# Performance work log

Hardware: AMD Instinct MI355X
Metric: run time of the kernel (lower is better)

The kernel has to match this reference:

```python
import jax, jax.numpy as jnp
import numpy as np

GAMMA = 0.99      # discount_factor
LAM = 0.95        # gae_decay
CLIP = 0.2        # clipping_param
LOG_2PI = float(np.log(2.0 * np.pi))

B, T, A = 512, 2048, 16


def setup_inputs() -> dict:
    key = jax.random.key(0)
    ks = jax.random.split(key, 8)
    rewards = jax.random.normal(ks[0], (B, T), dtype=jnp.float32)
    critic_out = jax.random.normal(ks[1], (B, T + 1), dtype=jnp.float32)
    mu = jax.random.normal(ks[2], (B, T, A), dtype=jnp.float32)
    sigma = jax.random.uniform(ks[3], (B, T, A), dtype=jnp.float32) * 0.5 + 0.5
    old_mu = jax.random.normal(ks[4], (B, T, A), dtype=jnp.float32)
    old_sigma = jax.random.uniform(ks[5], (B, T, A), dtype=jnp.float32) * 0.5 + 0.5
    actions = jax.random.normal(ks[6], (B, T, A), dtype=jnp.float32)
    dones = jax.random.randint(ks[7], (B, T), 0, 2, dtype=jnp.int32)
    return {"rewards": rewards, "critic_out": critic_out, "mu": mu, "sigma": sigma,
            "old_mu": old_mu, "old_sigma": old_sigma, "actions": actions, "dones": dones}


def _normal_log_prob(x, mu, sigma):
    return -jnp.log(sigma) - 0.5 * LOG_2PI - 0.5 * jnp.square((x - mu) / sigma)


def _gae(rewards, dones_f, critic_out):
    # td_residuals: rewards + gamma * V[1:] - V[:-1]   -> [B, T]
    td = rewards + GAMMA * critic_out[:, 1:] - critic_out[:, :-1]
    b, t = rewards.shape
    # Reversed recurrence: adv[t] = td[t] + gamma*lam*(1 - done[t+1]) * adv[t+1],
    # for t = T-2 .. 0; adv[T-1] stays 0 (matches original loop bounds).
    xs = (jnp.flip(td[:, : t - 1], axis=1).T,        # [T-1, B]
          jnp.flip(dones_f[:, 1:], axis=1).T)        # [T-1, B]

    def step(carry, x):
        td_t, d_t = x
        adv = td_t + GAMMA * LAM * (1.0 - d_t) * carry
        return adv, adv

    _, advs = jax.lax.scan(step, jnp.zeros((b,), rewards.dtype), xs)
    advs = jnp.flip(advs, axis=0).T                  # [B, T-1]
    return jnp.concatenate([advs, jnp.zeros((b, 1), rewards.dtype)], axis=1)


def reference(rewards, critic_out, mu, sigma, old_mu, old_sigma, actions, dones):
    dones_f = dones.astype(rewards.dtype)
    advantages = _gae(rewards, dones_f, critic_out)          # [B, T]
    lp = _normal_log_prob(actions, mu, sigma)                # [B, T, A]
    old_lp = _normal_log_prob(actions, old_mu, old_sigma)    # [B, T, A]
    ratio = jnp.exp(lp - old_lp)
    clipped = jnp.minimum(jnp.maximum(ratio, 1.0 + CLIP), 1.0 - CLIP)
    adv = advantages[..., None]                              # broadcast over action dim
    obj = jnp.minimum(adv * ratio, adv * clipped)
    entropy = jnp.log(sigma) + 0.5 + 0.5 * LOG_2PI           # Normal entropy, [B, T, A]
    return jnp.mean(obj) + entropy
```

## Files before the change

kernel.cpp:

```cpp
#include <hip/hip_runtime.h>
#include <math.h>

#define BB 512
#define TT 2048
#define AA 16
#define NTOT (512LL * 2048LL * 16LL)
#define GAMMA 0.99f
#define GLAM  0.9405f
#define ENTC  1.4189385332046727f

#define NB2 2048

__global__ __launch_bounds__(256) void gae_kernel(
    const float* __restrict__ rewards, const float* __restrict__ vout,
    const int* __restrict__ dones, float* __restrict__ adv)
{
    const int b   = blockIdx.x;
    const int tid = threadIdx.x;
    const float* rw = rewards + (size_t)b * TT;
    const float* V  = vout    + (size_t)b * (TT + 1);
    const int*   dn = dones   + (size_t)b * TT;
    float*       av = adv     + (size_t)b * TT;

    float ak[8], bk[8];
    float SA = 1.f, SB = 0.f;
    #pragma unroll
    for (int k = 0; k < 8; ++k) {
        int u = tid * 8 + k;
        float au, bu;
        if (u == 0) { au = 0.f; bu = 0.f; }
        else {
            int t = TT - 1 - u;
            bu = rw[t] + GAMMA * V[t + 1] - V[t];
            au = GLAM * (1.f - (float)dn[t + 1]);
        }
        ak[k] = au; bk[k] = bu;
        SB = au * SB + bu;
        SA = au * SA;
    }

    const int lane = tid & 63;
    const int wave = tid >> 6;

    #pragma unroll
    for (int off = 1; off < 64; off <<= 1) {
        float pA = __shfl_up(SA, off, 64);
        float pB = __shfl_up(SB, off, 64);
        if (lane >= off) { SB = SA * pB + SB; SA = SA * pA; }
    }

    __shared__ float wA[4], wB[4];
    if (lane == 63) { wA[wave] = SA; wB[wave] = SB; }
    __syncthreads();

    float PA = 1.f, PB = 0.f;
    for (int w = 0; w < wave; ++w) {
        float aw = wA[w], bw = wB[w];
        PB = aw * PB + bw;
        PA = aw * PA;
    }

    float EA = __shfl_up(SA, 1, 64);
    float EB = __shfl_up(SB, 1, 64);
    if (lane == 0) { EA = 1.f; EB = 0.f; }

    float x = EA * PB + EB;
    #pragma unroll
    for (int k = 0; k < 8; ++k) {
        x = ak[k] * x + bk[k];
        int u = tid * 8 + k;
        av[TT - 1 - u] = x;
    }
}

__device__ __forceinline__ float obj1(float x, float m, float s,
                                      float om, float os, float ad)
{
    float rs  = __builtin_amdgcn_rcpf(s);
    float ros = __builtin_amdgcn_rcpf(os);
    float z   = (x - m) * rs;
    float zo  = (x - om) * ros;
    float d   = 0.5f * (zo * zo - z * z);
    float ratio = os * rs * __expf(d);
    return fminf(ad * ratio, ad * 0.8f);
}

__global__ __launch_bounds__(256) void obj_kernel(
    const float* __restrict__ mu, const float* __restrict__ sigma,
    const float* __restrict__ old_mu, const float* __restrict__ old_sigma,
    const float* __restrict__ actions, const float* __restrict__ adv,
    double* __restrict__ partials)
{
    const int tid = threadIdx.x;
    const size_t gthread = (size_t)blockIdx.x * 256 + tid;
    const size_t stride  = (size_t)NB2 * 256;

    const float4* m4  = (const float4*)mu;
    const float4* s4  = (const float4*)sigma;
    const float4* om4 = (const float4*)old_mu;
    const float4* os4 = (const float4*)old_sigma;
    const float4* x4  = (const float4*)actions;

    double lsum = 0.0;
    #pragma unroll 2
    for (int it = 0; it < 8; ++it) {
        size_t v = gthread + (size_t)it * stride;
        float4 m  = m4[v];
        float4 s  = s4[v];
        float4 om = om4[v];
        float4 os = os4[v];
        float4 x  = x4[v];
        float ad  = adv[v >> 2];

        float o0 = obj1(x.x, m.x, s.x, om.x, os.x, ad);
        float o1 = obj1(x.y, m.y, s.y, om.y, os.y, ad);
        float o2 = obj1(x.z, m.z, s.z, om.z, os.z, ad);
        float o3 = obj1(x.w, m.w, s.w, om.w, os.w, ad);
        lsum += (double)o0 + (double)o1 + (double)o2 + (double)o3;
    }

    #pragma unroll
    for (int off = 32; off > 0; off >>= 1)
        lsum += __shfl_down(lsum, off, 64);

    __shared__ double wsum[4];
    const int lane = tid & 63, wave = tid >> 6;
    if (lane == 0) wsum[wave] = lsum;
    __syncthreads();
    if (tid == 0)
        partials[blockIdx.x] = wsum[0] + wsum[1] + wsum[2] + wsum[3];
}

__global__ __launch_bounds__(256) void reduce_kernel(
    const double* __restrict__ partials, float* __restrict__ meanOut)
{
    const int tid = threadIdx.x;
    double s = 0.0;
    for (int i = tid; i < NB2; i += 256) s += partials[i];
    #pragma unroll
    for (int off = 32; off > 0; off >>= 1)
        s += __shfl_down(s, off, 64);
    __shared__ double wsum[4];
    const int lane = tid & 63, wave = tid >> 6;
    if (lane == 0) wsum[wave] = s;
    __syncthreads();
    if (tid == 0) {
        double total = wsum[0] + wsum[1] + wsum[2] + wsum[3];
        meanOut[0] = (float)(total / (double)NTOT);
    }
}

__global__ __launch_bounds__(256) void out_kernel(
    const float* __restrict__ sigma, const float* __restrict__ meanPtr,
    float* __restrict__ out)
{
    const size_t v = (size_t)blockIdx.x * 256 + threadIdx.x;
    const float mean = *meanPtr;
    float4 s = ((const float4*)sigma)[v];
    float4 o;
    o.x = mean + __logf(s.x) + ENTC;
    o.y = mean + __logf(s.y) + ENTC;
    o.z = mean + __logf(s.z) + ENTC;
    o.w = mean + __logf(s.w) + ENTC;
    ((float4*)out)[v] = o;
}

extern "C" void kernel_launch(void* const* d_in, const int* in_sizes, int n_in,
                              void* d_out, int out_size, void* d_ws, size_t ws_size,
                              hipStream_t stream) {
    const float* rewards   = (const float*)d_in[0];
    const float* critic    = (const float*)d_in[1];
    const float* mu        = (const float*)d_in[2];
    const float* sigma     = (const float*)d_in[3];
    const float* old_mu    = (const float*)d_in[4];
    const float* old_sigma = (const float*)d_in[5];
    const float* actions   = (const float*)d_in[6];
    const int*   dones     = (const int*)d_in[7];
    float* out = (float*)d_out;

    char* ws = (char*)d_ws;
    float*  meanPtr  = (float*)ws;
    double* partials = (double*)(ws + 256);
    float*  adv      = (float*)(ws + 32768);

    gae_kernel<<<BB, 256, 0, stream>>>(rewards, critic, dones, adv);
    obj_kernel<<<NB2, 256, 0, stream>>>(mu, sigma, old_mu, old_sigma,
                                        actions, adv, partials);
    reduce_kernel<<<1, 256, 0, stream>>>(partials, meanPtr);
    out_kernel<<<(int)(NTOT / 4 / 256), 256, 0, stream>>>(sigma, meanPtr, out);
}
```

Measured before the change: 344.5 us.

## Vectorize GAE loads/stores, batch obj loads upfront, float accumulation, multi-item out kernel

The GAE kernel now reads rewards, critic values and dones as float4/int4 chunks and writes advantages as two float4 stores, replacing scalar strided accesses. The objective kernel doubles the grid to 4096 blocks with four items per thread. It issues all loads before any compute to raise memory-level parallelism, and it accumulates in four float registers instead of per-item double adds. The output kernel processes four float4 per thread over the same grid. Risks: the critic rows have a stride of 2049 floats, so the float4 loads from V are misaligned, and float accumulation loses some precision before the double reduction.

```diff
diff --git a/kernel.cpp b/kernel.cpp
--- a/kernel.cpp
+++ b/kernel.cpp
@@ -5,11 +5,14 @@
 #define TT 2048
 #define AA 16
 #define NTOT (512LL * 2048LL * 16LL)
+#define NV4  (NTOT / 4)
 #define GAMMA 0.99f
 #define GLAM  0.9405f
 #define ENTC  1.4189385332046727f
 
-#define NB2 2048
+#define NB2   4096
+#define ITER2 4
+#define S2    (NB2 * 256)
 
 __global__ __launch_bounds__(256) void gae_kernel(
     const float* __restrict__ rewards, const float* __restrict__ vout,
@@ -22,17 +25,31 @@
     const int*   dn = dones   + (size_t)b * TT;
     float*       av = adv     + (size_t)b * TT;
 
+    const int tb = (TT - 8) - 8 * tid;
+
+    const float4 r0 = ((const float4*)(rw + tb))[0];
+    const float4 r1 = ((const float4*)(rw + tb))[1];
+    const float4 v0 = ((const float4*)(V  + tb))[0];
+    const float4 v1 = ((const float4*)(V  + tb))[1];
+    const float  v8 = V[tb + 8];
+    const int4   d0 = ((const int4*)(dn + tb))[0];
+    const int4   d1 = ((const int4*)(dn + tb))[1];
+    const int    d8 = (tid > 0) ? dn[tb + 8] : 0;
+
+    float r_[8] = {r0.x, r0.y, r0.z, r0.w, r1.x, r1.y, r1.z, r1.w};
+    float v_[9] = {v0.x, v0.y, v0.z, v0.w, v1.x, v1.y, v1.z, v1.w, v8};
+    int   d_[9] = {d0.x, d0.y, d0.z, d0.w, d1.x, d1.y, d1.z, d1.w, d8};
+
     float ak[8], bk[8];
     float SA = 1.f, SB = 0.f;
     #pragma unroll
     for (int k = 0; k < 8; ++k) {
-        int u = tid * 8 + k;
+        const int j = 7 - k;
         float au, bu;
-        if (u == 0) { au = 0.f; bu = 0.f; }
+        if (tid == 0 && k == 0) { au = 0.f; bu = 0.f; }
         else {
-            int t = TT - 1 - u;
-            bu = rw[t] + GAMMA * V[t + 1] - V[t];
-            au = GLAM * (1.f - (float)dn[t + 1]);
+            bu = r_[j] + GAMMA * v_[j + 1] - v_[j];
+            au = GLAM * (1.f - (float)d_[j + 1]);
         }
         ak[k] = au; bk[k] = bu;
         SB = au * SB + bu;
@@ -65,12 +82,16 @@
     if (lane == 0) { EA = 1.f; EB = 0.f; }
 
     float x = EA * PB + EB;
+    float xv[8];
     #pragma unroll
     for (int k = 0; k < 8; ++k) {
         x = ak[k] * x + bk[k];
-        int u = tid * 8 + k;
-        av[TT - 1 - u] = x;
-    }
+        xv[k] = x;
+    }
+    float4 o0 = {xv[7], xv[6], xv[5], xv[4]};
+    float4 o1 = {xv[3], xv[2], xv[1], xv[0]};
+    ((float4*)(av + tb))[0] = o0;
+    ((float4*)(av + tb))[1] = o1;
 }
 
 __device__ __forceinline__ float obj1(float x, float m, float s,
@@ -92,8 +113,7 @@
     double* __restrict__ partials)
 {
     const int tid = threadIdx.x;
-    const size_t gthread = (size_t)blockIdx.x * 256 + tid;
-    const size_t stride  = (size_t)NB2 * 256;
+    const size_t g = (size_t)blockIdx.x * 256 + tid;
 
     const float4* m4  = (const float4*)mu;
     const float4* s4  = (const float4*)sigma;
@@ -101,23 +121,28 @@
     const float4* os4 = (const float4*)old_sigma;
     const float4* x4  = (const float4*)actions;
 
-    double lsum = 0.0;
-    #pragma unroll 2
-    for (int it = 0; it < 8; ++it) {
-        size_t v = gthread + (size_t)it * stride;
-        float4 m  = m4[v];
-        float4 s  = s4[v];
-        float4 om = om4[v];
-        float4 os = os4[v];
-        float4 x  = x4[v];
-        float ad  = adv[v >> 2];
-
-        float o0 = obj1(x.x, m.x, s.x, om.x, os.x, ad);
-        float o1 = obj1(x.y, m.y, s.y, om.y, os.y, ad);
-        float o2 = obj1(x.z, m.z, s.z, om.z, os.z, ad);
-        float o3 = obj1(x.w, m.w, s.w, om.w, os.w, ad);
-        lsum += (double)o0 + (double)o1 + (double)o2 + (double)o3;
-    }
+    float4 m[ITER2], s[ITER2], om[ITER2], os[ITER2], x[ITER2];
+    float ad[ITER2];
+    #pragma unroll
+    for (int k = 0; k < ITER2; ++k) {
+        size_t v = g + (size_t)k * S2;
+        m[k]  = m4[v];
+        s[k]  = s4[v];
+        om[k] = om4[v];
+        os[k] = os4[v];
+        x[k]  = x4[v];
+        ad[k] = adv[v >> 2];
+    }
+
+    float a0 = 0.f, a1 = 0.f, a2 = 0.f, a3 = 0.f;
+    #pragma unroll
+    for (int k = 0; k < ITER2; ++k) {
+        a0 += obj1(x[k].x, m[k].x, s[k].x, om[k].x, os[k].x, ad[k]);
+        a1 += obj1(x[k].y, m[k].y, s[k].y, om[k].y, os[k].y, ad[k]);
+        a2 += obj1(x[k].z, m[k].z, s[k].z, om[k].z, os[k].z, ad[k]);
+        a3 += obj1(x[k].w, m[k].w, s[k].w, om[k].w, os[k].w, ad[k]);
+    }
+    double lsum = ((double)a0 + (double)a1) + ((double)a2 + (double)a3);
 
     #pragma unroll
     for (int off = 32; off > 0; off >>= 1)
@@ -154,15 +179,21 @@
     const float* __restrict__ sigma, const float* __restrict__ meanPtr,
     float* __restrict__ out)
 {
-    const size_t v = (size_t)blockIdx.x * 256 + threadIdx.x;
-    const float mean = *meanPtr;
-    float4 s = ((const float4*)sigma)[v];
-    float4 o;
-    o.x = mean + __logf(s.x) + ENTC;
-    o.y = mean + __logf(s.y) + ENTC;
-    o.z = mean + __logf(s.z) + ENTC;
-    o.w = mean + __logf(s.w) + ENTC;
-    ((float4*)out)[v] = o;
+    const size_t g = (size_t)blockIdx.x * 256 + threadIdx.x;
+    const float mean = meanPtr[0];
+    const float4* s4 = (const float4*)sigma;
+    float4* o4 = (float4*)out;
+    #pragma unroll
+    for (int k = 0; k < ITER2; ++k) {
+        size_t v = g + (size_t)k * S2;
+        float4 s = s4[v];
+        float4 o;
+        o.x = mean + __logf(s.x) + ENTC;
+        o.y = mean + __logf(s.y) + ENTC;
+        o.z = mean + __logf(s.z) + ENTC;
+        o.w = mean + __logf(s.w) + ENTC;
+        o4[v] = o;
+    }
 }
 
 extern "C" void kernel_launch(void* const* d_in, const int* in_sizes, int n_in,
@@ -181,11 +212,11 @@
     char* ws = (char*)d_ws;
     float*  meanPtr  = (float*)ws;
     double* partials = (double*)(ws + 256);
-    float*  adv      = (float*)(ws + 32768);
+    float*  adv      = (float*)(ws + 65536);
 
     gae_kernel<<<BB, 256, 0, stream>>>(rewards, critic, dones, adv);
     obj_kernel<<<NB2, 256, 0, stream>>>(mu, sigma, old_mu, old_sigma,
                                         actions, adv, partials);
     reduce_kernel<<<1, 256, 0, stream>>>(partials, meanPtr);
-    out_kernel<<<(int)(NTOT / 4 / 256), 256, 0, stream>>>(sigma, meanPtr, out);
-}
+    out_kernel<<<NB2, 256, 0, stream>>>(sigma, meanPtr, out);
+}
```

New measurement: 346.3 us. About the same (+0.5%).
